# Kernel tuning notes

Measured on AMD Instinct MI355X. Metric: run time of the kernel, lower is better.

Reference implementation:

```python
import jax, jax.numpy as jnp
import numpy as np

TEMPERATURE_F = 0.5  # temperature_f from __init__


def setup_inputs() -> dict:
    key = jax.random.key(0)
    k1, k2 = jax.random.split(key)
    B, D = 4096, 512
    h_i = jax.random.normal(k1, (B, D), dtype=jnp.float32)
    h_j = jax.random.normal(k2, (B, D), dtype=jnp.float32)
    return {"h_i": h_i, "h_j": h_j}


def reference(h_i, h_j) -> jnp.ndarray:
    # NT-Xent loss (forward_private). N = 2*batch_size.
    B = h_i.shape[0]
    N = 2 * B
    h = jnp.concatenate([h_i, h_j], axis=0)          # [N, D]
    sim = (h @ h.T) / TEMPERATURE_F                   # [N, N]

    # Positive pairs: sim[i, i+B] and sim[i+B, i]
    sim_i_j = jnp.diagonal(sim, offset=B)             # [B]
    sim_j_i = jnp.diagonal(sim, offset=-B)            # [B]
    pos = jnp.concatenate([sim_i_j, sim_j_i], axis=0)  # [N]

    # Original builds logits = [pos | negatives] where negatives are the row of
    # sim with the diagonal and the positive entry removed, and labels are 0.
    # Cross-entropy per row = -pos_i + logsumexp(pos_i, negatives_i)
    #                       = -pos_i + logsumexp over row i of sim excluding the
    #                         diagonal (the positive entry equals pos_i, so the
    #                         set of logsumexp'd values is identical).
    neg_inf = jnp.finfo(sim.dtype).min
    diag = jnp.eye(N, dtype=bool)
    sim_masked = jnp.where(diag, neg_inf, sim)        # exclude self-similarity
    lse = jax.nn.logsumexp(sim_masked, axis=1)        # [N]

    loss = jnp.sum(lse - pos) / N                     # CE sum reduction, / N
    return loss
```

## Files before the change

kernel.cpp:

```cpp
#include <hip/hip_runtime.h>
#include <hip/hip_bf16.h>
#include <float.h>

#define BN_ 4096
#define DD  512
#define NN  8192
#define SCALE 2.0f
#define NTILE 2080

typedef unsigned short u16;
typedef __attribute__((ext_vector_type(8))) short short8;
typedef __attribute__((ext_vector_type(4))) float floatx4;

struct alignas(8) U16x4 { u16 x, y, z, w; };

__device__ __forceinline__ u16 f2bf(float f) {
    union { float f; unsigned u; } c; c.f = f;
    unsigned u = c.u;
    unsigned r = (u + 0x7fffu + ((u >> 16) & 1u)) >> 16;
    return (u16)r;
}

__device__ __forceinline__ void async_copy16(const u16* g, u16* l) {
    __builtin_amdgcn_global_load_lds(
        (const __attribute__((address_space(1))) void*)g,
        (__attribute__((address_space(3))) void*)l, 16, 0, 0);
}

__global__ __launch_bounds__(256) void convert_pos_kernel(const float* __restrict__ hi,
                                                          const float* __restrict__ hj,
                                                          u16* __restrict__ H,
                                                          float* __restrict__ Pos,
                                                          float* __restrict__ out) {
    __shared__ float red[4];
    int t = blockIdx.x * 256 + threadIdx.x;
    int e = t * 4;
    const int BD = BN_ * DD;
    float4 a = *(const float4*)(hi + e);
    float4 b = *(const float4*)(hj + e);
    U16x4 oa, ob;
    oa.x = f2bf(a.x); oa.y = f2bf(a.y); oa.z = f2bf(a.z); oa.w = f2bf(a.w);
    ob.x = f2bf(b.x); ob.y = f2bf(b.y); ob.z = f2bf(b.z); ob.w = f2bf(b.w);
    *(U16x4*)(H + e) = oa;
    *(U16x4*)(H + BD + e) = ob;
    float dot = a.x * b.x + a.y * b.y + a.z * b.z + a.w * b.w;
#pragma unroll
    for (int msk = 1; msk < 64; msk <<= 1) dot += __shfl_xor(dot, msk);
    int lane = threadIdx.x & 63, wid = threadIdx.x >> 6;
    if (lane == 0) red[wid] = dot;
    __syncthreads();
    if (threadIdx.x == 0) {
        Pos[blockIdx.x] = red[0] + red[1] + red[2] + red[3];
        if (blockIdx.x == 0) *out = 0.0f;
    }
}

__global__ __launch_bounds__(256, 4) void gram_kernel(const u16* __restrict__ H,
                                                      float* __restrict__ Mpart,
                                                      float* __restrict__ Spart) {
    __shared__ u16 As[128 * 64];
    __shared__ u16 Bs[128 * 64];

    float* Rm = (float*)&As[0];
    float* Rs = Rm + 256;
    float* Cm = Rs + 256;
    float* Cs = Cm + 256;

    const int tid  = threadIdx.x;
    const int lane = tid & 63;
    const int wid  = tid >> 6;
    const int quad = lane >> 4;
    const int ln15 = lane & 15;
    const int wr = wid >> 1, wc = wid & 1;

    int t = ((int)blockIdx.x & 7) * (NTILE / 8) + ((int)blockIdx.x >> 3);

    int bi = (int)((sqrtf(8.0f * (float)t + 1.0f) - 1.0f) * 0.5f);
    while ((bi + 1) * (bi + 2) / 2 <= t) bi++;
    while (bi * (bi + 1) / 2 > t) bi--;
    const int bj = t - bi * (bi + 1) / 2;
    const bool diag = (bi == bj);
    const int biBase = bi * 128, bjBase = bj * 128;

    const u16* srcA[4];
    int ldsOff[4];
#pragma unroll
    for (int j = 0; j < 4; j++) {
        int c   = j * 256 + tid;
        int row = c >> 3;
        int kc  = (c & 7) ^ (row & 7);
        srcA[j]   = H + (size_t)(biBase + row) * DD + kc * 8;
        ldsOff[j] = c * 8;
    }
    const ptrdiff_t dB = (ptrdiff_t)(bjBase - biBase) * DD;

    floatx4 acc[4][4];
#pragma unroll
    for (int i = 0; i < 4; i++)
#pragma unroll
        for (int j = 0; j < 4; j++) acc[i][j] = (floatx4)0.0f;

    for (int k0 = 0; k0 < DD; k0 += 64) {
#pragma unroll
        for (int j = 0; j < 4; j++) async_copy16(srcA[j] + k0,      &As[ldsOff[j]]);
#pragma unroll
        for (int j = 0; j < 4; j++) async_copy16(srcA[j] + dB + k0, &Bs[ldsOff[j]]);
        __syncthreads();

#pragma unroll
        for (int kk = 0; kk < 2; kk++) {
            int ck = kk * 4 + quad;
            short8 a[4], b[4];
#pragma unroll
            for (int tm = 0; tm < 4; tm++) {
                int r = wr * 64 + tm * 16 + ln15;
                a[tm] = *(const short8*)&As[(r * 8 + (ck ^ (r & 7))) * 8];
            }
#pragma unroll
            for (int tn = 0; tn < 4; tn++) {
                int r = wc * 64 + tn * 16 + ln15;
                b[tn] = *(const short8*)&Bs[(r * 8 + (ck ^ (r & 7))) * 8];
            }
#pragma unroll
            for (int tm = 0; tm < 4; tm++)
#pragma unroll
                for (int tn = 0; tn < 4; tn++)
                    acc[tm][tn] = __builtin_amdgcn_mfma_f32_16x16x32_bf16(
                        a[tm], b[tn], acc[tm][tn], 0, 0, 0);
        }
        __syncthreads();
    }

#pragma unroll
    for (int tm = 0; tm < 4; tm++)
#pragma unroll
        for (int tn = 0; tn < 4; tn++)
#pragma unroll
            for (int r = 0; r < 4; r++) {
                float v = SCALE * acc[tm][tn][r];
                if (diag) {
                    int lrow = wr * 64 + tm * 16 + quad * 4 + r;
                    int lcol = wc * 64 + tn * 16 + ln15;
                    if (lrow == lcol) v = -FLT_MAX;
                }
                acc[tm][tn][r] = v;
            }

#pragma unroll
    for (int tm = 0; tm < 4; tm++) {
#pragma unroll
        for (int r = 0; r < 4; r++) {
            float vmax = -FLT_MAX;
#pragma unroll
            for (int tn = 0; tn < 4; tn++) vmax = fmaxf(vmax, acc[tm][tn][r]);
#pragma unroll
            for (int msk = 1; msk < 16; msk <<= 1)
                vmax = fmaxf(vmax, __shfl_xor(vmax, msk));
            float s = 0.0f;
#pragma unroll
            for (int tn = 0; tn < 4; tn++) s += __expf(acc[tm][tn][r] - vmax);
#pragma unroll
            for (int msk = 1; msk < 16; msk <<= 1) s += __shfl_xor(s, msk);
            if (ln15 == 0) {
                int x = wr * 64 + tm * 16 + quad * 4 + r;
                Rm[wc * 128 + x] = vmax; Rs[wc * 128 + x] = s;
            }
        }
    }

    if (!diag) {
#pragma unroll
        for (int tn = 0; tn < 4; tn++) {
            float cm = -FLT_MAX;
#pragma unroll
            for (int tm = 0; tm < 4; tm++)
#pragma unroll
                for (int r = 0; r < 4; r++) cm = fmaxf(cm, acc[tm][tn][r]);
            cm = fmaxf(cm, __shfl_xor(cm, 16));
            cm = fmaxf(cm, __shfl_xor(cm, 32));
            float s = 0.0f;
#pragma unroll
            for (int tm = 0; tm < 4; tm++)
#pragma unroll
                for (int r = 0; r < 4; r++) s += __expf(acc[tm][tn][r] - cm);
            s += __shfl_xor(s, 16);
            s += __shfl_xor(s, 32);
            if (quad == 0) {
                int y = wc * 64 + tn * 16 + ln15;
                Cm[wr * 128 + y] = cm; Cs[wr * 128 + y] = s;
            }
        }
    }
    __syncthreads();

    if (tid < 128) {
        float m0 = Rm[tid], m1 = Rm[128 + tid];
        float s0 = Rs[tid], s1 = Rs[128 + tid];
        float m = fmaxf(m0, m1);
        float s = s0 * __expf(m0 - m) + s1 * __expf(m1 - m);
        Mpart[(size_t)bj * NN + biBase + tid] = m;
        Spart[(size_t)bj * NN + biBase + tid] = s;
    } else if (!diag) {
        int y = tid - 128;
        float m0 = Cm[y], m1 = Cm[128 + y];
        float s0 = Cs[y], s1 = Cs[128 + y];
        float m = fmaxf(m0, m1);
        float s = s0 * __expf(m0 - m) + s1 * __expf(m1 - m);
        Mpart[(size_t)bi * NN + bjBase + y] = m;
        Spart[(size_t)bi * NN + bjBase + y] = s;
    }
}

__global__ __launch_bounds__(256) void lse_kernel(const float* __restrict__ Mpart,
                                                  const float* __restrict__ Spart,
                                                  const float* __restrict__ Pos,
                                                  float* __restrict__ out) {
    __shared__ float sm[4][64], ss[4][64];
    __shared__ float red[256];
    int tid = threadIdx.x;
    int wid = tid >> 6, lane = tid & 63;
    int r = blockIdx.x * 64 + lane;
    float m = -FLT_MAX, s = 0.0f;
#pragma unroll
    for (int i = 0; i < 16; i++) {
        int c = wid * 16 + i;
        float mc = Mpart[(size_t)c * NN + r];
        float sc = Spart[(size_t)c * NN + r];
        float mn = fmaxf(m, mc);
        s = s * __expf(m - mn) + sc * __expf(mc - mn);
        m = mn;
    }
    sm[wid][lane] = m; ss[wid][lane] = s;
    __syncthreads();
    float v = 0.0f;
    if (tid < 64) {
        float m0 = sm[0][tid], m1 = sm[1][tid], m2 = sm[2][tid], m3 = sm[3][tid];
        float mm = fmaxf(fmaxf(m0, m1), fmaxf(m2, m3));
        float sa = ss[0][tid] * __expf(m0 - mm) + ss[1][tid] * __expf(m1 - mm)
                 + ss[2][tid] * __expf(m2 - mm) + ss[3][tid] * __expf(m3 - mm);
        v = mm + logf(sa);
        if (tid < 16) v += -4.0f * Pos[blockIdx.x * 16 + tid];
    }
    red[tid] = v;
    __syncthreads();
    for (int st = 128; st > 0; st >>= 1) {
        if (tid < st) red[tid] += red[tid + st];
        __syncthreads();
    }
    if (tid == 0) atomicAdd(out, red[0] * (1.0f / (float)NN));
}

extern "C" void kernel_launch(void* const* d_in, const int* in_sizes, int n_in,
                              void* d_out, int out_size, void* d_ws, size_t ws_size,
                              hipStream_t stream) {
    const float* hi = (const float*)d_in[0];
    const float* hj = (const float*)d_in[1];
    float* out = (float*)d_out;

    u16*   H     = (u16*)d_ws;
    float* Mpart = (float*)((char*)d_ws + (size_t)8 * 1024 * 1024);
    float* Spart = (float*)((char*)d_ws + (size_t)10 * 1024 * 1024);
    float* Pos   = (float*)((char*)d_ws + (size_t)12 * 1024 * 1024);

    convert_pos_kernel<<<2048, 256, 0, stream>>>(hi, hj, H, Pos, out);

    gram_kernel<<<NTILE, 256, 0, stream>>>(H, Mpart, Spart);

    lse_kernel<<<128, 256, 0, stream>>>(Mpart, Spart, Pos, out);
}
```

Baseline: 131.0 us.

## Split gram tile across eight waves with 64x32 per-wave subtiles

The Gram kernel goes from 256 to 512 threads per block. The 128x128 tile is now divided into a 2x4 grid of waves, each computing a 64x32 subtile, which halves accumulator registers per wave and spreads the loads and MFMA work over more waves. The row and column softmax reductions and the LDS scratch layout are reworked to merge four column-wave partials for rows. The aim is more latency hiding per block, at the cost of more A-fragment LDS reads per MFMA and heavier barriers.

```diff
diff --git a/kernel.cpp b/kernel.cpp
--- a/kernel.cpp
+++ b/kernel.cpp
@@ -55,15 +55,15 @@
     }
 }
 
-__global__ __launch_bounds__(256, 4) void gram_kernel(const u16* __restrict__ H,
+__global__ __launch_bounds__(512, 4) void gram_kernel(const u16* __restrict__ H,
                                                       float* __restrict__ Mpart,
                                                       float* __restrict__ Spart) {
     __shared__ u16 As[128 * 64];
     __shared__ u16 Bs[128 * 64];
 
     float* Rm = (float*)&As[0];
-    float* Rs = Rm + 256;
-    float* Cm = Rs + 256;
+    float* Rs = Rm + 512;
+    float* Cm = Rs + 512;
     float* Cs = Cm + 256;
 
     const int tid  = threadIdx.x;
@@ -71,7 +71,8 @@
     const int wid  = tid >> 6;
     const int quad = lane >> 4;
     const int ln15 = lane & 15;
-    const int wr = wid >> 1, wc = wid & 1;
+    const int wr = wid >> 2;
+    const int wc = wid & 3;
 
     int t = ((int)blockIdx.x & 7) * (NTILE / 8) + ((int)blockIdx.x >> 3);
 
@@ -82,51 +83,45 @@
     const bool diag = (bi == bj);
     const int biBase = bi * 128, bjBase = bj * 128;
 
-    const u16* srcA[4];
-    int ldsOff[4];
-#pragma unroll
-    for (int j = 0; j < 4; j++) {
-        int c   = j * 256 + tid;
-        int row = c >> 3;
-        int kc  = (c & 7) ^ (row & 7);
-        srcA[j]   = H + (size_t)(biBase + row) * DD + kc * 8;
-        ldsOff[j] = c * 8;
-    }
+    const int rowT = tid >> 3;
+    const int kcT  = ((tid & 7) ^ (rowT & 7)) * 8;
+    const u16* __restrict__ srcA0 = H + (size_t)(biBase + rowT) * DD + kcT;
     const ptrdiff_t dB = (ptrdiff_t)(bjBase - biBase) * DD;
-
-    floatx4 acc[4][4];
+    const ptrdiff_t dJ = (ptrdiff_t)64 * DD;
+    u16* ldsA0 = &As[tid * 8];
+    u16* ldsB0 = &Bs[tid * 8];
+
+    floatx4 acc[4][2];
 #pragma unroll
     for (int i = 0; i < 4; i++)
 #pragma unroll
-        for (int j = 0; j < 4; j++) acc[i][j] = (floatx4)0.0f;
+        for (int j = 0; j < 2; j++) acc[i][j] = (floatx4)0.0f;
 
     for (int k0 = 0; k0 < DD; k0 += 64) {
-#pragma unroll
-        for (int j = 0; j < 4; j++) async_copy16(srcA[j] + k0,      &As[ldsOff[j]]);
-#pragma unroll
-        for (int j = 0; j < 4; j++) async_copy16(srcA[j] + dB + k0, &Bs[ldsOff[j]]);
+        async_copy16(srcA0 + k0,           ldsA0);
+        async_copy16(srcA0 + dJ + k0,      ldsA0 + 4096);
+        async_copy16(srcA0 + dB + k0,      ldsB0);
+        async_copy16(srcA0 + dB + dJ + k0, ldsB0 + 4096);
         __syncthreads();
 
 #pragma unroll
         for (int kk = 0; kk < 2; kk++) {
             int ck = kk * 4 + quad;
-            short8 a[4], b[4];
+            short8 b[2];
+#pragma unroll
+            for (int tn = 0; tn < 2; tn++) {
+                int r = wc * 32 + tn * 16 + ln15;
+                b[tn] = *(const short8*)&Bs[(r * 8 + (ck ^ (r & 7))) * 8];
+            }
 #pragma unroll
             for (int tm = 0; tm < 4; tm++) {
                 int r = wr * 64 + tm * 16 + ln15;
-                a[tm] = *(const short8*)&As[(r * 8 + (ck ^ (r & 7))) * 8];
-            }
-#pragma unroll
-            for (int tn = 0; tn < 4; tn++) {
-                int r = wc * 64 + tn * 16 + ln15;
-                b[tn] = *(const short8*)&Bs[(r * 8 + (ck ^ (r & 7))) * 8];
-            }
-#pragma unroll
-            for (int tm = 0; tm < 4; tm++)
-#pragma unroll
-                for (int tn = 0; tn < 4; tn++)
+                short8 a = *(const short8*)&As[(r * 8 + (ck ^ (r & 7))) * 8];
+#pragma unroll
+                for (int tn = 0; tn < 2; tn++)
                     acc[tm][tn] = __builtin_amdgcn_mfma_f32_16x16x32_bf16(
-                        a[tm], b[tn], acc[tm][tn], 0, 0, 0);
+                        a, b[tn], acc[tm][tn], 0, 0, 0);
+            }
         }
         __syncthreads();
     }
@@ -134,13 +129,13 @@
 #pragma unroll
     for (int tm = 0; tm < 4; tm++)
 #pragma unroll
-        for (int tn = 0; tn < 4; tn++)
+        for (int tn = 0; tn < 2; tn++)
 #pragma unroll
             for (int r = 0; r < 4; r++) {
                 float v = SCALE * acc[tm][tn][r];
                 if (diag) {
                     int lrow = wr * 64 + tm * 16 + quad * 4 + r;
-                    int lcol = wc * 64 + tn * 16 + ln15;
+                    int lcol = wc * 32 + tn * 16 + ln15;
                     if (lrow == lcol) v = -FLT_MAX;
                 }
                 acc[tm][tn][r] = v;
@@ -150,15 +145,11 @@
     for (int tm = 0; tm < 4; tm++) {
 #pragma unroll
         for (int r = 0; r < 4; r++) {
-            float vmax = -FLT_MAX;
-#pragma unroll
-            for (int tn = 0; tn < 4; tn++) vmax = fmaxf(vmax, acc[tm][tn][r]);
+            float vmax = fmaxf(acc[tm][0][r], acc[tm][1][r]);
 #pragma unroll
             for (int msk = 1; msk < 16; msk <<= 1)
                 vmax = fmaxf(vmax, __shfl_xor(vmax, msk));
-            float s = 0.0f;
-#pragma unroll
-            for (int tn = 0; tn < 4; tn++) s += __expf(acc[tm][tn][r] - vmax);
+            float s = __expf(acc[tm][0][r] - vmax) + __expf(acc[tm][1][r] - vmax);
 #pragma unroll
             for (int msk = 1; msk < 16; msk <<= 1) s += __shfl_xor(s, msk);
             if (ln15 == 0) {
@@ -170,7 +161,7 @@
 
     if (!diag) {
 #pragma unroll
-        for (int tn = 0; tn < 4; tn++) {
+        for (int tn = 0; tn < 2; tn++) {
             float cm = -FLT_MAX;
 #pragma unroll
             for (int tm = 0; tm < 4; tm++)
@@ -186,7 +177,7 @@
             s += __shfl_xor(s, 16);
             s += __shfl_xor(s, 32);
             if (quad == 0) {
-                int y = wc * 64 + tn * 16 + ln15;
+                int y = wc * 32 + tn * 16 + ln15;
                 Cm[wr * 128 + y] = cm; Cs[wr * 128 + y] = s;
             }
         }
@@ -194,19 +185,18 @@
     __syncthreads();
 
     if (tid < 128) {
-        float m0 = Rm[tid], m1 = Rm[128 + tid];
-        float s0 = Rs[tid], s1 = Rs[128 + tid];
-        float m = fmaxf(m0, m1);
-        float s = s0 * __expf(m0 - m) + s1 * __expf(m1 - m);
-        Mpart[(size_t)bj * NN + biBase + tid] = m;
+        float m0 = Rm[tid], m1 = Rm[128 + tid], m2 = Rm[256 + tid], m3 = Rm[384 + tid];
+        float mm = fmaxf(fmaxf(m0, m1), fmaxf(m2, m3));
+        float s = Rs[tid] * __expf(m0 - mm) + Rs[128 + tid] * __expf(m1 - mm)
+                + Rs[256 + tid] * __expf(m2 - mm) + Rs[384 + tid] * __expf(m3 - mm);
+        Mpart[(size_t)bj * NN + biBase + tid] = mm;
         Spart[(size_t)bj * NN + biBase + tid] = s;
-    } else if (!diag) {
+    } else if (tid < 256 && !diag) {
         int y = tid - 128;
         float m0 = Cm[y], m1 = Cm[128 + y];
-        float s0 = Cs[y], s1 = Cs[128 + y];
-        float m = fmaxf(m0, m1);
-        float s = s0 * __expf(m0 - m) + s1 * __expf(m1 - m);
-        Mpart[(size_t)bi * NN + bjBase + y] = m;
+        float mm = fmaxf(m0, m1);
+        float s = Cs[y] * __expf(m0 - mm) + Cs[128 + y] * __expf(m1 - mm);
+        Mpart[(size_t)bi * NN + bjBase + y] = mm;
         Spart[(size_t)bi * NN + bjBase + y] = s;
     }
 }
@@ -264,7 +254,7 @@
 
     convert_pos_kernel<<<2048, 256, 0, stream>>>(hi, hj, H, Pos, out);
 
-    gram_kernel<<<NTILE, 256, 0, stream>>>(H, Mpart, Spart);
+    gram_kernel<<<NTILE, 512, 0, stream>>>(H, Mpart, Spart);
 
     lse_kernel<<<128, 256, 0, stream>>>(Mpart, Spart, Pos, out);
 }
```

Result: slower. 133.9 us (+2.2%).

## Process two column tiles per block sharing the A tile with 512 threads

Applied to the files above, without the earlier changes.

Each block now computes two 128x128 tiles of the upper-triangular Gram matrix (same row block, adjacent column blocks). Eight waves are used, and the A tile in LDS is shared between the two sub-tiles. The block count drops from 2080 to 1056, and a new cumulative-index mapping handles rows with an odd tile count. This cuts redundant global and LDS loads of the A tile. In exchange it uses more LDS per block, which may lower occupancy, and leaves some blocks half-idle on single-tile rows.

```diff
diff --git a/kernel.cpp b/kernel.cpp
--- a/kernel.cpp
+++ b/kernel.cpp
@@ -6,7 +6,7 @@
 #define DD  512
 #define NN  8192
 #define SCALE 2.0f
-#define NTILE 2080
+#define NBLK 1056
 
 typedef unsigned short u16;
 typedef __attribute__((ext_vector_type(8))) short short8;
@@ -55,44 +55,49 @@
     }
 }
 
-__global__ __launch_bounds__(256, 4) void gram_kernel(const u16* __restrict__ H,
+#define CUM(b) (((b) & 1) ? (((b) + 1) * ((b) + 1) / 4) : ((b) * ((b) + 2) / 4))
+
+__global__ __launch_bounds__(512, 4) void gram_kernel(const u16* __restrict__ H,
                                                       float* __restrict__ Mpart,
                                                       float* __restrict__ Spart) {
     __shared__ u16 As[128 * 64];
-    __shared__ u16 Bs[128 * 64];
+    __shared__ u16 Bs[2][128 * 64];
 
     float* Rm = (float*)&As[0];
-    float* Rs = Rm + 256;
-    float* Cm = Rs + 256;
-    float* Cs = Cm + 256;
+    float* Rs = Rm + 512;
+    float* Cm = Rs + 512;
+    float* Cs = Cm + 512;
 
     const int tid  = threadIdx.x;
     const int lane = tid & 63;
     const int wid  = tid >> 6;
     const int quad = lane >> 4;
     const int ln15 = lane & 15;
-    const int wr = wid >> 1, wc = wid & 1;
-
-    int t = ((int)blockIdx.x & 7) * (NTILE / 8) + ((int)blockIdx.x >> 3);
-
-    int bi = (int)((sqrtf(8.0f * (float)t + 1.0f) - 1.0f) * 0.5f);
-    while ((bi + 1) * (bi + 2) / 2 <= t) bi++;
-    while (bi * (bi + 1) / 2 > t) bi--;
-    const int bj = t - bi * (bi + 1) / 2;
-    const bool diag = (bi == bj);
-    const int biBase = bi * 128, bjBase = bj * 128;
-
-    const u16* srcA[4];
-    int ldsOff[4];
-#pragma unroll
-    for (int j = 0; j < 4; j++) {
-        int c   = j * 256 + tid;
-        int row = c >> 3;
-        int kc  = (c & 7) ^ (row & 7);
-        srcA[j]   = H + (size_t)(biBase + row) * DD + kc * 8;
-        ldsOff[j] = c * 8;
-    }
-    const ptrdiff_t dB = (ptrdiff_t)(bjBase - biBase) * DD;
+    const int sub  = wid >> 2;
+    const int wr = (wid >> 1) & 1;
+    const int wc = wid & 1;
+
+    int p = ((int)blockIdx.x & 7) * (NBLK / 8) + ((int)blockIdx.x >> 3);
+
+    int bi = (int)(2.0f * sqrtf((float)p + 1.0f));
+    if (bi > 63) bi = 63;
+    while (CUM(bi + 1) <= p) bi++;
+    while (CUM(bi) > p) bi--;
+    const int q   = p - CUM(bi);
+    const int bj0 = 2 * q;
+    const int bj1 = (bj0 + 1 <= bi) ? bj0 + 1 : bj0;
+    const bool single = (bj1 == bj0);
+    const int biBase = bi * 128;
+    const int bjS = sub ? bj1 : bj0;
+    const bool diagS = (bjS == bi);
+
+    const int rowT = tid >> 3;
+    const int kcT  = ((tid & 7) ^ (rowT & 7)) * 8;
+    const u16* __restrict__ src = H + (size_t)(biBase + rowT) * DD + kcT;
+    const ptrdiff_t dB0 = (ptrdiff_t)(bj0 * 128 - biBase) * DD;
+    const ptrdiff_t dB1 = (ptrdiff_t)(bj1 * 128 - biBase) * DD;
+    const ptrdiff_t dJ  = (ptrdiff_t)64 * DD;
+    const int d0 = tid * 8;
 
     floatx4 acc[4][4];
 #pragma unroll
@@ -101,32 +106,33 @@
         for (int j = 0; j < 4; j++) acc[i][j] = (floatx4)0.0f;
 
     for (int k0 = 0; k0 < DD; k0 += 64) {
-#pragma unroll
-        for (int j = 0; j < 4; j++) async_copy16(srcA[j] + k0,      &As[ldsOff[j]]);
-#pragma unroll
-        for (int j = 0; j < 4; j++) async_copy16(srcA[j] + dB + k0, &Bs[ldsOff[j]]);
+        async_copy16(src + k0,            &As[d0]);
+        async_copy16(src + dJ + k0,       &As[d0 + 4096]);
+        async_copy16(src + dB0 + k0,      &Bs[0][d0]);
+        async_copy16(src + dB0 + dJ + k0, &Bs[0][d0 + 4096]);
+        async_copy16(src + dB1 + k0,      &Bs[1][d0]);
+        async_copy16(src + dB1 + dJ + k0, &Bs[1][d0 + 4096]);
         __syncthreads();
 
+        const u16* __restrict__ Bsub = Bs[sub];
 #pragma unroll
         for (int kk = 0; kk < 2; kk++) {
             int ck = kk * 4 + quad;
-            short8 a[4], b[4];
+            short8 b[4];
+#pragma unroll
+            for (int tn = 0; tn < 4; tn++) {
+                int r = wc * 64 + tn * 16 + ln15;
+                b[tn] = *(const short8*)&Bsub[(r * 8 + (ck ^ (r & 7))) * 8];
+            }
 #pragma unroll
             for (int tm = 0; tm < 4; tm++) {
                 int r = wr * 64 + tm * 16 + ln15;
-                a[tm] = *(const short8*)&As[(r * 8 + (ck ^ (r & 7))) * 8];
-            }
-#pragma unroll
-            for (int tn = 0; tn < 4; tn++) {
-                int r = wc * 64 + tn * 16 + ln15;
-                b[tn] = *(const short8*)&Bs[(r * 8 + (ck ^ (r & 7))) * 8];
-            }
-#pragma unroll
-            for (int tm = 0; tm < 4; tm++)
+                short8 a = *(const short8*)&As[(r * 8 + (ck ^ (r & 7))) * 8];
 #pragma unroll
                 for (int tn = 0; tn < 4; tn++)
                     acc[tm][tn] = __builtin_amdgcn_mfma_f32_16x16x32_bf16(
-                        a[tm], b[tn], acc[tm][tn], 0, 0, 0);
+                        a, b[tn], acc[tm][tn], 0, 0, 0);
+            }
         }
         __syncthreads();
     }
@@ -138,7 +144,7 @@
 #pragma unroll
             for (int r = 0; r < 4; r++) {
                 float v = SCALE * acc[tm][tn][r];
-                if (diag) {
+                if (diagS) {
                     int lrow = wr * 64 + tm * 16 + quad * 4 + r;
                     int lcol = wc * 64 + tn * 16 + ln15;
                     if (lrow == lcol) v = -FLT_MAX;
@@ -163,12 +169,13 @@
             for (int msk = 1; msk < 16; msk <<= 1) s += __shfl_xor(s, msk);
             if (ln15 == 0) {
                 int x = wr * 64 + tm * 16 + quad * 4 + r;
-                Rm[wc * 128 + x] = vmax; Rs[wc * 128 + x] = s;
-            }
-        }
-    }
-
-    if (!diag) {
+                Rm[sub * 256 + wc * 128 + x] = vmax;
+                Rs[sub * 256 + wc * 128 + x] = s;
+            }
+        }
+    }
+
+    if (!diagS) {
 #pragma unroll
         for (int tn = 0; tn < 4; tn++) {
             float cm = -FLT_MAX;
@@ -187,27 +194,45 @@
             s += __shfl_xor(s, 32);
             if (quad == 0) {
                 int y = wc * 64 + tn * 16 + ln15;
-                Cm[wr * 128 + y] = cm; Cs[wr * 128 + y] = s;
-            }
-        }
-    }
-    __syncthreads();
-
-    if (tid < 128) {
-        float m0 = Rm[tid], m1 = Rm[128 + tid];
-        float s0 = Rs[tid], s1 = Rs[128 + tid];
-        float m = fmaxf(m0, m1);
-        float s = s0 * __expf(m0 - m) + s1 * __expf(m1 - m);
-        Mpart[(size_t)bj * NN + biBase + tid] = m;
-        Spart[(size_t)bj * NN + biBase + tid] = s;
-    } else if (!diag) {
-        int y = tid - 128;
-        float m0 = Cm[y], m1 = Cm[128 + y];
-        float s0 = Cs[y], s1 = Cs[128 + y];
-        float m = fmaxf(m0, m1);
-        float s = s0 * __expf(m0 - m) + s1 * __expf(m1 - m);
-        Mpart[(size_t)bi * NN + bjBase + y] = m;
-        Spart[(size_t)bi * NN + bjBase + y] = s;
+                Cm[sub * 256 + wr * 128 + y] = cm;
+                Cs[sub * 256 + wr * 128 + y] = s;
+            }
+        }
+    }
+    __syncthreads();
+
+    const int r5 = tid & 127;
+    const int seg = tid >> 7;
+    if (seg == 0) {
+        float m0 = Rm[r5], m1 = Rm[128 + r5];
+        float mm = fmaxf(m0, m1);
+        float s = Rs[r5] * __expf(m0 - mm) + Rs[128 + r5] * __expf(m1 - mm);
+        Mpart[(size_t)bj0 * NN + biBase + r5] = mm;
+        Spart[(size_t)bj0 * NN + biBase + r5] = s;
+    } else if (seg == 1) {
+        if (bj0 != bi) {
+            float m0 = Cm[r5], m1 = Cm[128 + r5];
+            float mm = fmaxf(m0, m1);
+            float s = Cs[r5] * __expf(m0 - mm) + Cs[128 + r5] * __expf(m1 - mm);
+            Mpart[(size_t)bi * NN + bj0 * 128 + r5] = mm;
+            Spart[(size_t)bi * NN + bj0 * 128 + r5] = s;
+        }
+    } else if (seg == 2) {
+        if (!single) {
+            float m0 = Rm[256 + r5], m1 = Rm[384 + r5];
+            float mm = fmaxf(m0, m1);
+            float s = Rs[256 + r5] * __expf(m0 - mm) + Rs[384 + r5] * __expf(m1 - mm);
+            Mpart[(size_t)bj1 * NN + biBase + r5] = mm;
+            Spart[(size_t)bj1 * NN + biBase + r5] = s;
+        }
+    } else {
+        if (!single && bj1 != bi) {
+            float m0 = Cm[256 + r5], m1 = Cm[384 + r5];
+            float mm = fmaxf(m0, m1);
+            float s = Cs[256 + r5] * __expf(m0 - mm) + Cs[384 + r5] * __expf(m1 - mm);
+            Mpart[(size_t)bi * NN + bj1 * 128 + r5] = mm;
+            Spart[(size_t)bi * NN + bj1 * 128 + r5] = s;
+        }
     }
 }
 
@@ -264,7 +289,7 @@
 
     convert_pos_kernel<<<2048, 256, 0, stream>>>(hi, hj, H, Pos, out);
 
-    gram_kernel<<<NTILE, 256, 0, stream>>>(H, Mpart, Spart);
+    gram_kernel<<<NBLK, 512, 0, stream>>>(H, Mpart, Spart);
 
     lse_kernel<<<128, 256, 0, stream>>>(Mpart, Spart, Pos, out);
 }
```

Measured after the change: 135.8 us. 1.04x slower.
